# Optimization experiments

Hardware: AMD Instinct MI355X
Metric: run time of the kernel (lower is better)

The kernel has to match this reference:

```python
import jax, jax.numpy as jnp
import numpy as np

N_NODES = 100000
N_EDGES = 3200000
IN_DIM, HID, OUT = 512, 256, 64


def setup_inputs() -> dict:
    key = jax.random.key(0)
    k1, k2, k3, k4, k5, k6 = jax.random.split(key, 6)
    x = jax.random.normal(k1, (N_NODES, IN_DIM), dtype=jnp.float32)
    edge_src = jax.random.randint(k2, (N_EDGES,), 0, N_NODES, dtype=jnp.int32)
    edge_dst = jax.random.randint(k3, (N_EDGES,), 0, N_NODES, dtype=jnp.int32)
    edge_val = jax.random.uniform(k4, (N_EDGES,), dtype=jnp.float32)
    # glorot init as in the original `glorot([input_dim, output_dim])`
    w1 = jax.random.normal(k5, (IN_DIM, HID), dtype=jnp.float32) * np.sqrt(2.0 / (IN_DIM + HID))
    w2 = jax.random.normal(k6, (HID, OUT), dtype=jnp.float32) * np.sqrt(2.0 / (HID + OUT))
    return {"x": x, "edge_src": edge_src, "edge_dst": edge_dst,
            "edge_val": edge_val, "w1": w1, "w2": w2}


def _spmm(edge_src, edge_dst, edge_val, dense):
    # support @ dense : out[i] = sum_j A[i,j] * dense[j], A given as COO edges
    msgs = edge_val[:, None] * dense[edge_dst]            # [E, D] gather
    return jax.ops.segment_sum(msgs, edge_src, num_segments=N_NODES)  # scatter-add


def reference(x, edge_src, edge_dst, edge_val, w1, w2):
    # Layer 1: pre_sup = X @ W1 ; support = A @ pre_sup ; relu (no bias)
    h = jax.nn.relu(_spmm(edge_src, edge_dst, edge_val, x @ w1))  # [N, HID]
    # Layer 2: identity activation
    logits = _spmm(edge_src, edge_dst, edge_val, h @ w2)          # [N, OUT]
    return logits
```

## Files before the change

kernel.cpp:

```cpp
#include <hip/hip_runtime.h>

#define NN 100000
#define NE 3200000
#define IN_DIM 512
#define HID 256
#define OUTD 64
#define NB 196
#define CAP 20480
#define EPB 3125

typedef _Float16 f16x8 __attribute__((ext_vector_type(8)));
typedef float f32x4 __attribute__((ext_vector_type(4)));

__device__ __forceinline__ void async_copy16(void* lds, const void* g) {
    __builtin_amdgcn_global_load_lds(
        (const __attribute__((address_space(1))) void*)g,
        (__attribute__((address_space(3))) void*)lds, 16, 0, 0);
}

__device__ __forceinline__ void dq4(int w, float m, float* a) {
    int lo = (w & 0x00ff00ff) | 0x64006400;
    int hi = ((w >> 8) & 0x00ff00ff) | 0x64006400;
    asm("v_fma_mix_f32 %0, %1, %2, %0 op_sel:[0,0,0] op_sel_hi:[1,0,0]" : "+v"(a[0]) : "v"(lo), "v"(m));
    asm("v_fma_mix_f32 %0, %1, %2, %0 op_sel:[0,0,0] op_sel_hi:[1,0,0]" : "+v"(a[1]) : "v"(hi), "v"(m));
    asm("v_fma_mix_f32 %0, %1, %2, %0 op_sel:[1,0,0] op_sel_hi:[1,0,0]" : "+v"(a[2]) : "v"(lo), "v"(m));
    asm("v_fma_mix_f32 %0, %1, %2, %0 op_sel:[1,0,0] op_sel_hi:[1,0,0]" : "+v"(a[3]) : "v"(hi), "v"(m));
}


__global__ void prep_kernel(const float* __restrict__ w1, const float* __restrict__ w2,
                            _Float16* __restrict__ w1t, _Float16* __restrict__ w2t,
                            int* __restrict__ cursor) {
    int idx = blockIdx.x * blockDim.x + threadIdx.x;
    if (idx < NB) cursor[idx] = idx * CAP;
    if (idx < IN_DIM * HID) {
        int k = idx / HID, n = idx % HID;
        w1t[(size_t)n * IN_DIM + k] = (_Float16)w1[idx];
    } else if (idx < IN_DIM * HID + HID * OUTD) {
        int j = idx - IN_DIM * HID;
        int k = j / OUTD, n = j % OUTD;
        w2t[(size_t)n * HID + k] = (_Float16)w2[j];
    }
}


__global__ __launch_bounds__(256) void bin_kernel(const int* __restrict__ src,
                                                  const int* __restrict__ dst,
                                                  const float* __restrict__ val,
                                                  int* __restrict__ cursor,
                                                  int2* __restrict__ pairs_tmp,
                                                  int E) {
    __shared__ int s_src[EPB];
    __shared__ int s_dst[EPB];
    __shared__ int s_val[EPB];
    __shared__ int hist[NB];
    __shared__ int base[NB];
    const int t = threadIdx.x;
    const int lo = blockIdx.x * EPB;
    const int cnt = min(E - lo, EPB);
    for (int i = t; i < NB; i += 256) hist[i] = 0;
    for (int i = t; i < cnt; i += 256) {
        s_src[i] = src[lo + i];
        s_dst[i] = dst[lo + i];
        s_val[i] = __float_as_int(val[lo + i]);
    }
    __syncthreads();
    for (int i = t; i < cnt; i += 256) atomicAdd(&hist[s_src[i] >> 9], 1);
    __syncthreads();
    for (int i = t; i < NB; i += 256) {
        base[i] = atomicAdd(&cursor[i], hist[i]);
        hist[i] = 0;
    }
    __syncthreads();
    for (int i = t; i < cnt; i += 256) {
        int s = s_src[i];
        int b = s >> 9;
        int l = atomicAdd(&hist[b], 1);
        int pos = base[b] + l;
        pairs_tmp[pos] = make_int2(s_dst[i] | ((s & 511) << 20), s_val[i]);
    }
}


__global__ void bucket_scan_kernel(const int* __restrict__ cursor,
                                   int* __restrict__ bbase, int* __restrict__ offs) {
    __shared__ int sz[NB];
    int t = threadIdx.x;
    if (t < NB) sz[t] = cursor[t] - t * CAP;
    __syncthreads();
    if (t == 0) {
        int acc = 0;
        for (int i = 0; i < NB; ++i) { bbase[i] = acc; acc += sz[i]; }
        bbase[NB] = acc;
        offs[NN] = acc;
    }
}


#define CSR_LDS 18432
__global__ __launch_bounds__(1024) void csr_kernel(const int* __restrict__ cursor,
                                                   const int* __restrict__ bbase,
                                                   const int2* __restrict__ pairs_tmp,
                                                   const float* __restrict__ scales,
                                                   int* __restrict__ offs,
                                                   int2* __restrict__ pairs) {
    __shared__ int sx[CSR_LDS];
    __shared__ int sv[CSR_LDS];
    __shared__ int cnt[512];
    __shared__ int wsum[8];
    const int b = blockIdx.x;
    const int t = threadIdx.x;
    const int s0 = b << 9;
    const int base = bbase[b];
    const int n_b = cursor[b] - b * CAP;
    const int tlo = b * CAP;
    if (t < 512) cnt[t] = 0;
    __syncthreads();
    for (int i = t; i < n_b; i += 1024) {
        int2 pv = pairs_tmp[tlo + i];
        sx[i] = pv.x;
        sv[i] = pv.y;
        atomicAdd(&cnt[((unsigned)pv.x) >> 20], 1);
    }
    __syncthreads();
    int my = 0, incl = 0;
    if (t < 512) {
        my = cnt[t];
        incl = my;
        #pragma unroll
        for (int d = 1; d < 64; d <<= 1) {
            int y = __shfl_up(incl, d);
            if ((t & 63) >= d) incl += y;
        }
        if ((t & 63) == 63) wsum[t >> 6] = incl;
    }
    __syncthreads();
    if (t == 0) {
        int acc = 0;
        #pragma unroll
        for (int i = 0; i < 8; ++i) { int v = wsum[i]; wsum[i] = acc; acc += v; }
    }
    __syncthreads();
    if (t < 512) {
        int excl = base + incl - my + wsum[t >> 6];
        int s = s0 + t;
        if (s < NN) offs[s] = excl;
        cnt[t] = excl;
    }
    __syncthreads();
    for (int i = t; i < n_b; i += 1024) {
        int x = sx[i];
        int so = ((unsigned)x) >> 20;
        int p = atomicAdd(&cnt[so], 1);
        int dst = x & 0xFFFFF;
        float v = __int_as_float(sv[i]) * scales[dst];
        pairs[p] = make_int2(dst, __float_as_int(v));
    }
}


__global__ __launch_bounds__(256) void gemm1_f32a(const float* __restrict__ A,
                                                  const _Float16* __restrict__ Bt,
                                                  unsigned char* __restrict__ qC,
                                                  float* __restrict__ scales,
                                                  int M) {
    __shared__ float    As[2][64 * 32];
    __shared__ _Float16 Bs[2][256 * 32];
    __shared__ float    rmaxl[2][64];
    const int tid  = threadIdx.x;
    const int lane = tid & 63;
    const int wave = tid >> 6;
    const int wm = wave >> 1, wn = wave & 1;
    const int m0 = blockIdx.x * 64;

    f32x4 acc[2][8];
    #pragma unroll
    for (int i = 0; i < 2; ++i)
        #pragma unroll
        for (int j = 0; j < 8; ++j) acc[i][j] = (f32x4){0.f, 0.f, 0.f, 0.f};

    auto stage = [&](int b, int k0) {
        #pragma unroll
        for (int it = 0; it < 2; ++it) {
            int i = it * 256 + tid;
            int r = i >> 3;
            int cl = (i & 7) ^ (r & 7);
            int gr = m0 + r; if (gr >= M) gr = M - 1;
            async_copy16((char*)As[b] + i * 16, A + (size_t)gr * IN_DIM + k0 + cl * 4);
        }
        #pragma unroll
        for (int it = 0; it < 4; ++it) {
            int i = it * 256 + tid;
            int r = i >> 2;
            int cl = (i & 3) ^ (r & 3);
            async_copy16((char*)Bs[b] + i * 16, Bt + (size_t)r * IN_DIM + k0 + cl * 8);
        }
    };

    stage(0, 0);
    __syncthreads();

    int cur = 0;
    const int kc = lane >> 4;
    for (int t = 0; t < IN_DIM / 32; ++t) {
        if (t + 1 < IN_DIM / 32) stage(cur ^ 1, (t + 1) * 32);

        f16x8 af[2];
        #pragma unroll
        for (int m = 0; m < 2; ++m) {
            int r = wm * 32 + m * 16 + (lane & 15);
            int p0 = (2 * kc) ^ (r & 7);
            int p1 = (2 * kc + 1) ^ (r & 7);
            f32x4 c0 = *(const f32x4*)((const char*)As[cur] + r * 128 + p0 * 16);
            f32x4 c1 = *(const f32x4*)((const char*)As[cur] + r * 128 + p1 * 16);
            f16x8 v = { (_Float16)c0[0], (_Float16)c0[1], (_Float16)c0[2], (_Float16)c0[3],
                        (_Float16)c1[0], (_Float16)c1[1], (_Float16)c1[2], (_Float16)c1[3] };
            af[m] = v;
        }
        f16x8 bf[8];
        #pragma unroll
        for (int n = 0; n < 8; ++n) {
            int r = wn * 128 + n * 16 + (lane & 15);
            bf[n] = *(const f16x8*)((const char*)Bs[cur] + r * 64 + ((kc ^ (r & 3)) * 16));
        }
        #pragma unroll
        for (int m = 0; m < 2; ++m)
            #pragma unroll
            for (int n = 0; n < 8; ++n)
                acc[m][n] = __builtin_amdgcn_mfma_f32_16x16x32_f16(af[m], bf[n], acc[m][n], 0, 0, 0);

        __syncthreads();
        cur ^= 1;
    }

    #pragma unroll
    for (int m = 0; m < 2; ++m)
        #pragma unroll
        for (int r = 0; r < 4; ++r) {
            float mm = 0.f;
            #pragma unroll
            for (int n = 0; n < 8; ++n) mm = fmaxf(mm, fabsf(acc[m][n][r]));
            #pragma unroll
            for (int d = 1; d < 16; d <<= 1) mm = fmaxf(mm, __shfl_xor(mm, d));
            if ((lane & 15) == 0)
                rmaxl[wn][wm * 32 + m * 16 + kc * 4 + r] = mm;
        }
    __syncthreads();
    #pragma unroll
    for (int m = 0; m < 2; ++m)
        #pragma unroll
        for (int r = 0; r < 4; ++r) {
            int lrow = wm * 32 + m * 16 + kc * 4 + r;
            int row = m0 + lrow;
            float full = fmaxf(fmaxf(rmaxl[0][lrow], rmaxl[1][lrow]), 1e-12f);
            float inv = 127.0f / full;
            if (row < M) {
                #pragma unroll
                for (int n = 0; n < 8; ++n) {
                    int col = wn * 128 + n * 16 + (lane & 15);
                    qC[(size_t)row * HID + col] =
                        (unsigned char)(__float2int_rn(acc[m][n][r] * inv) + 128);
                }
                if (wn == 0 && (lane & 15) == 0) scales[row] = full * (1.0f / 127.0f);
            }
        }
}


__global__ __launch_bounds__(256) void spmm_relu_mm2(const int* __restrict__ offs,
                                                     const int2* __restrict__ pairs,
                                                     const unsigned char* __restrict__ qpre,
                                                     const float* __restrict__ scales,
                                                     const _Float16* __restrict__ w2t,
                                                     unsigned char* __restrict__ qh2,
                                                     float* __restrict__ ratio2, int n) {
    __shared__ __align__(16) char hl_raw[16 * 528];
    __shared__ float rmax2[4][16];
    const int tid  = threadIdx.x;
    const int lane = tid & 63;
    const int wid  = tid >> 6;
    const int par  = lane >> 4;
    const int fl   = lane & 15;
    const int nbase = blockIdx.x * 16;
    const unsigned char* qbase = qpre + fl * 16;

    #pragma unroll 1
    for (int i = 0; i < 4; ++i) {
        const int node = nbase + wid * 4 + i;
        const int beg = offs[node], end = offs[node + 1];
        float a[16] = {};
        float msum = 0.f;
        int k = beg;
        for (; k + 16 <= end; k += 16) {
            int2 pr[4];
            #pragma unroll
            for (int j = 0; j < 4; ++j) pr[j] = pairs[k + 4 * j + par];
            int4 qv[4];
            #pragma unroll
            for (int j = 0; j < 4; ++j)
                qv[j] = *(const int4*)(qbase + (size_t)pr[j].x * HID);
            #pragma unroll
            for (int j = 0; j < 4; ++j) {
                float m = __int_as_float(pr[j].y);
                msum += m;
                dq4(qv[j].x, m, a + 0);
                dq4(qv[j].y, m, a + 4);
                dq4(qv[j].z, m, a + 8);
                dq4(qv[j].w, m, a + 12);
            }
        }
        if (k < end) {
            int2 pr[4];
            float m_[4];
            #pragma unroll
            for (int j = 0; j < 4; ++j) {
                int idx = k + 4 * j + par;
                int cidx = idx < end ? idx : end - 1;
                pr[j] = pairs[cidx];
                m_[j] = idx < end ? __int_as_float(pr[j].y) : 0.f;
            }
            int4 qv[4];
            #pragma unroll
            for (int j = 0; j < 4; ++j)
                qv[j] = *(const int4*)(qbase + (size_t)pr[j].x * HID);
            #pragma unroll
            for (int j = 0; j < 4; ++j) {
                float m = m_[j];
                msum += m;
                dq4(qv[j].x, m, a + 0);
                dq4(qv[j].y, m, a + 4);
                dq4(qv[j].z, m, a + 8);
                dq4(qv[j].w, m, a + 12);
            }
        }
        #pragma unroll
        for (int q = 0; q < 16; ++q) {
            a[q] += __shfl_xor(a[q], 16);
            a[q] += __shfl_xor(a[q], 32);
        }
        msum += __shfl_xor(msum, 16);
        msum += __shfl_xor(msum, 32);
        if (par == 0) {
            float bias = 1152.f * msum;
            f16x8 o0, o1;
            #pragma unroll
            for (int q = 0; q < 8; ++q) {
                o0[q] = (_Float16)fmaxf(a[q] - bias, 0.f);
                o1[q] = (_Float16)fmaxf(a[8 + q] - bias, 0.f);
            }
            char* bp = hl_raw + (wid * 4 + i) * 528 + fl * 16;
            *(f16x8*)bp         = o0;
            *(f16x8*)(bp + 256) = o1;
        }
    }
    __syncthreads();

    const int r  = lane & 15;
    const int kc = lane >> 4;
    f32x4 acc = (f32x4){0.f, 0.f, 0.f, 0.f};
    #pragma unroll
    for (int kk = 0; kk < 8; ++kk) {
        int c = kk * 4 + kc;
        f16x8 af = *(const f16x8*)(hl_raw + r * 528 + ((c & 1) << 8) + ((c >> 1) << 4));
        f16x8 bf = *(const f16x8*)(w2t + (size_t)(wid * 16 + r) * HID + kk * 32 + kc * 8);
        acc = __builtin_amdgcn_mfma_f32_16x16x32_f16(af, bf, acc, 0, 0, 0);
    }
    float mxv[4];
    #pragma unroll
    for (int j = 0; j < 4; ++j) {
        float mm = fabsf(acc[j]);
        #pragma unroll
        for (int d = 1; d < 16; d <<= 1) mm = fmaxf(mm, __shfl_xor(mm, d));
        mxv[j] = mm;
    }
    if (r == 0) {
        #pragma unroll
        for (int j = 0; j < 4; ++j) rmax2[wid][kc * 4 + j] = mxv[j];
    }
    __syncthreads();
    #pragma unroll
    for (int j = 0; j < 4; ++j) {
        int ln = kc * 4 + j;
        int node = nbase + ln;
        float full = fmaxf(fmaxf(fmaxf(rmax2[0][ln], rmax2[1][ln]),
                                 fmaxf(rmax2[2][ln], rmax2[3][ln])), 1e-12f);
        qh2[(size_t)node * OUTD + wid * 16 + r] =
            (unsigned char)(__float2int_rn(acc[j] * (127.0f / full)) + 128);
        if (wid == 0 && r == 0)
            ratio2[node] = full * (1.0f / 127.0f) / scales[node];
    }
}


__global__ __launch_bounds__(256) void spmm64_q(const int* __restrict__ offs,
                                                const int2* __restrict__ pairs,
                                                const unsigned char* __restrict__ qh2,
                                                const float* __restrict__ ratio2,
                                                float* __restrict__ out, int n) {
    int node = blockIdx.x * 4 + (threadIdx.x >> 6);
    if (node >= n) return;
    int lane = threadIdx.x & 63;
    int par = lane >> 2;
    int fl  = lane & 3;
    int beg = offs[node], end = offs[node + 1];
    const unsigned char* qbase = qh2 + fl * 16;
    float a[16] = {};
    float msum = 0.f;
    int k = beg;
    for (; k + 32 <= end; k += 32) {
        int2 pr[2];
        #pragma unroll
        for (int j = 0; j < 2; ++j) pr[j] = pairs[k + 16 * j + par];
        float rt[2];
        #pragma unroll
        for (int j = 0; j < 2; ++j) rt[j] = ratio2[pr[j].x];
        int4 qv[2];
        #pragma unroll
        for (int j = 0; j < 2; ++j)
            qv[j] = *(const int4*)(qbase + (size_t)pr[j].x * OUTD);
        #pragma unroll
        for (int j = 0; j < 2; ++j) {
            float m = __int_as_float(pr[j].y) * rt[j];
            msum += m;
            dq4(qv[j].x, m, a + 0);
            dq4(qv[j].y, m, a + 4);
            dq4(qv[j].z, m, a + 8);
            dq4(qv[j].w, m, a + 12);
        }
    }
    if (k < end) {
        int2 pr[2];
        float m_[2];
        #pragma unroll
        for (int j = 0; j < 2; ++j) {
            int idx = k + 16 * j + par;
            int cidx = idx < end ? idx : end - 1;
            pr[j] = pairs[cidx];
            m_[j] = idx < end ? __int_as_float(pr[j].y) * ratio2[pr[j].x] : 0.f;
        }
        int4 qv[2];
        #pragma unroll
        for (int j = 0; j < 2; ++j)
            qv[j] = *(const int4*)(qbase + (size_t)pr[j].x * OUTD);
        #pragma unroll
        for (int j = 0; j < 2; ++j) {
            float m = m_[j];
            msum += m;
            dq4(qv[j].x, m, a + 0);
            dq4(qv[j].y, m, a + 4);
            dq4(qv[j].z, m, a + 8);
            dq4(qv[j].w, m, a + 12);
        }
    }
    #pragma unroll
    for (int q = 0; q < 16; ++q) {
        a[q] += __shfl_xor(a[q], 4);
        a[q] += __shfl_xor(a[q], 8);
        a[q] += __shfl_xor(a[q], 16);
        a[q] += __shfl_xor(a[q], 32);
    }
    msum += __shfl_xor(msum, 4);
    msum += __shfl_xor(msum, 8);
    msum += __shfl_xor(msum, 16);
    msum += __shfl_xor(msum, 32);
    if (par == 0) {
        float bias = 1152.f * msum;
        float* ob = out + (size_t)node * OUTD + fl * 16;
        #pragma unroll
        for (int c = 0; c < 4; ++c) {
            float4 o = make_float4(a[4 * c] - bias, a[4 * c + 1] - bias,
                                   a[4 * c + 2] - bias, a[4 * c + 3] - bias);
            *(float4*)(ob + 4 * c) = o;
        }
    }
}


extern "C" void kernel_launch(void* const* d_in, const int* in_sizes, int n_in,
                              void* d_out, int out_size, void* d_ws, size_t ws_size,
                              hipStream_t stream) {
    const float* x    = (const float*)d_in[0];
    const int*   esrc = (const int*)d_in[1];
    const int*   edst = (const int*)d_in[2];
    const float* eval = (const float*)d_in[3];
    const float* w1   = (const float*)d_in[4];
    const float* w2   = (const float*)d_in[5];
    float* out = (float*)d_out;

    char* ws = (char*)d_ws;
    unsigned char* qpre   = (unsigned char*)(ws + 0);
    unsigned char* qh2    = (unsigned char*)(ws + 25600000);
    float*        scales  = (float*)(ws + 32000000);
    float*        ratio2  = (float*)(ws + 32400000);
    int2*         pairs   = (int2*)(ws + 32800000);
    int2*         pairs_t = (int2*)(ws + 58400000);
    int*          cursor  = (int*)(ws + 90512640);
    int*          bbase   = (int*)(ws + 90513664);
    int*          offs    = (int*)(ws + 90514688);
    _Float16*     w1t     = (_Float16*)(ws + 90914816);
    _Float16*     w2t     = (_Float16*)(ws + 91176960);

    prep_kernel<<<(IN_DIM * HID + HID * OUTD + 255) / 256, 256, 0, stream>>>(w1, w2, w1t, w2t, cursor);

    bin_kernel<<<1024, 256, 0, stream>>>(esrc, edst, eval, cursor, pairs_t, NE);

    bucket_scan_kernel<<<1, 256, 0, stream>>>(cursor, bbase, offs);

    gemm1_f32a<<<(NN + 63) / 64, 256, 0, stream>>>(x, w1t, qpre, scales, NN);

    csr_kernel<<<NB, 1024, 0, stream>>>(cursor, bbase, pairs_t, scales, offs, pairs);

    spmm_relu_mm2<<<NN / 16, 256, 0, stream>>>(offs, pairs, qpre, scales, w2t, qh2, ratio2, NN);

    spmm64_q<<<(NN + 3) / 4, 256, 0, stream>>>(offs, pairs, qh2, ratio2, out, NN);
}
```

Baseline: 385.3 us.

## Store layer-2 intermediate as fp16 and drop LDS staging in bin/csr kernels

Layer-2 features are now written as fp16 prescaled by the inverse of the per-node layer-1 scale, replacing the int8 quantization with a per-row max reduction, a ratio array and a bias correction. The final SpMM gathers 16-byte fp16 chunks with 8 lanes per row and needs no bias subtraction, which also removes a block-wide sync in the fused kernel. The cost is twice the gather bytes per edge in the last SpMM. Separately, bin_kernel and csr_kernel stop staging dst/val in LDS and reread global memory instead, which cuts LDS use (more occupancy) at the price of extra global reads.

Result: slower. 397.3 us (+3.1%).

```diff
diff --git a/kernel.cpp b/kernel.cpp
--- a/kernel.cpp
+++ b/kernel.cpp
@@ -25,6 +25,11 @@
     asm("v_fma_mix_f32 %0, %1, %2, %0 op_sel:[0,0,0] op_sel_hi:[1,0,0]" : "+v"(a[1]) : "v"(hi), "v"(m));
     asm("v_fma_mix_f32 %0, %1, %2, %0 op_sel:[1,0,0] op_sel_hi:[1,0,0]" : "+v"(a[2]) : "v"(lo), "v"(m));
     asm("v_fma_mix_f32 %0, %1, %2, %0 op_sel:[1,0,0] op_sel_hi:[1,0,0]" : "+v"(a[3]) : "v"(hi), "v"(m));
+}
+
+__device__ __forceinline__ void dqh2(int w, float m, float* a0, float* a1) {
+    asm("v_fma_mix_f32 %0, %1, %2, %0 op_sel:[0,0,0] op_sel_hi:[1,0,0]" : "+v"(*a0) : "v"(w), "v"(m));
+    asm("v_fma_mix_f32 %0, %1, %2, %0 op_sel:[1,0,0] op_sel_hi:[1,0,0]" : "+v"(*a1) : "v"(w), "v"(m));
 }
 
 
@@ -51,19 +56,13 @@
                                                   int2* __restrict__ pairs_tmp,
                                                   int E) {
     __shared__ int s_src[EPB];
-    __shared__ int s_dst[EPB];
-    __shared__ int s_val[EPB];
     __shared__ int hist[NB];
     __shared__ int base[NB];
     const int t = threadIdx.x;
     const int lo = blockIdx.x * EPB;
     const int cnt = min(E - lo, EPB);
     for (int i = t; i < NB; i += 256) hist[i] = 0;
-    for (int i = t; i < cnt; i += 256) {
-        s_src[i] = src[lo + i];
-        s_dst[i] = dst[lo + i];
-        s_val[i] = __float_as_int(val[lo + i]);
-    }
+    for (int i = t; i < cnt; i += 256) s_src[i] = src[lo + i];
     __syncthreads();
     for (int i = t; i < cnt; i += 256) atomicAdd(&hist[s_src[i] >> 9], 1);
     __syncthreads();
@@ -77,7 +76,7 @@
         int b = s >> 9;
         int l = atomicAdd(&hist[b], 1);
         int pos = base[b] + l;
-        pairs_tmp[pos] = make_int2(s_dst[i] | ((s & 511) << 20), s_val[i]);
+        pairs_tmp[pos] = make_int2(dst[lo + i] | ((s & 511) << 20), __float_as_int(val[lo + i]));
     }
 }
 
@@ -97,15 +96,12 @@
 }
 
 
-#define CSR_LDS 18432
 __global__ __launch_bounds__(1024) void csr_kernel(const int* __restrict__ cursor,
                                                    const int* __restrict__ bbase,
                                                    const int2* __restrict__ pairs_tmp,
                                                    const float* __restrict__ scales,
                                                    int* __restrict__ offs,
                                                    int2* __restrict__ pairs) {
-    __shared__ int sx[CSR_LDS];
-    __shared__ int sv[CSR_LDS];
     __shared__ int cnt[512];
     __shared__ int wsum[8];
     const int b = blockIdx.x;
@@ -116,12 +112,8 @@
     const int tlo = b * CAP;
     if (t < 512) cnt[t] = 0;
     __syncthreads();
-    for (int i = t; i < n_b; i += 1024) {
-        int2 pv = pairs_tmp[tlo + i];
-        sx[i] = pv.x;
-        sv[i] = pv.y;
-        atomicAdd(&cnt[((unsigned)pv.x) >> 20], 1);
-    }
+    for (int i = t; i < n_b; i += 1024)
+        atomicAdd(&cnt[((unsigned)pairs_tmp[tlo + i].x) >> 20], 1);
     __syncthreads();
     int my = 0, incl = 0;
     if (t < 512) {
@@ -149,11 +141,11 @@
     }
     __syncthreads();
     for (int i = t; i < n_b; i += 1024) {
-        int x = sx[i];
-        int so = ((unsigned)x) >> 20;
+        int2 pv = pairs_tmp[tlo + i];
+        int so = ((unsigned)pv.x) >> 20;
         int p = atomicAdd(&cnt[so], 1);
-        int dst = x & 0xFFFFF;
-        float v = __int_as_float(sv[i]) * scales[dst];
+        int dst = pv.x & 0xFFFFF;
+        float v = __int_as_float(pv.y) * scales[dst];
         pairs[p] = make_int2(dst, __float_as_int(v));
     }
 }
@@ -272,10 +264,8 @@
                                                      const unsigned char* __restrict__ qpre,
                                                      const float* __restrict__ scales,
                                                      const _Float16* __restrict__ w2t,
-                                                     unsigned char* __restrict__ qh2,
-                                                     float* __restrict__ ratio2, int n) {
+                                                     _Float16* __restrict__ h2s, int n) {
     __shared__ __align__(16) char hl_raw[16 * 528];
-    __shared__ float rmax2[4][16];
     const int tid  = threadIdx.x;
     const int lane = tid & 63;
     const int wid  = tid >> 6;
@@ -365,113 +355,80 @@
         f16x8 bf = *(const f16x8*)(w2t + (size_t)(wid * 16 + r) * HID + kk * 32 + kc * 8);
         acc = __builtin_amdgcn_mfma_f32_16x16x32_f16(af, bf, acc, 0, 0, 0);
     }
-    float mxv[4];
     #pragma unroll
     for (int j = 0; j < 4; ++j) {
-        float mm = fabsf(acc[j]);
-        #pragma unroll
-        for (int d = 1; d < 16; d <<= 1) mm = fmaxf(mm, __shfl_xor(mm, d));
-        mxv[j] = mm;
-    }
-    if (r == 0) {
-        #pragma unroll
-        for (int j = 0; j < 4; ++j) rmax2[wid][kc * 4 + j] = mxv[j];
-    }
-    __syncthreads();
-    #pragma unroll
-    for (int j = 0; j < 4; ++j) {
-        int ln = kc * 4 + j;
-        int node = nbase + ln;
-        float full = fmaxf(fmaxf(fmaxf(rmax2[0][ln], rmax2[1][ln]),
-                                 fmaxf(rmax2[2][ln], rmax2[3][ln])), 1e-12f);
-        qh2[(size_t)node * OUTD + wid * 16 + r] =
-            (unsigned char)(__float2int_rn(acc[j] * (127.0f / full)) + 128);
-        if (wid == 0 && r == 0)
-            ratio2[node] = full * (1.0f / 127.0f) / scales[node];
+        int node = nbase + kc * 4 + j;
+        float inv = 1.0f / scales[node];
+        h2s[(size_t)node * OUTD + wid * 16 + r] = (_Float16)(acc[j] * inv);
     }
 }
 
 
 __global__ __launch_bounds__(256) void spmm64_q(const int* __restrict__ offs,
                                                 const int2* __restrict__ pairs,
-                                                const unsigned char* __restrict__ qh2,
-                                                const float* __restrict__ ratio2,
+                                                const _Float16* __restrict__ h2s,
                                                 float* __restrict__ out, int n) {
     int node = blockIdx.x * 4 + (threadIdx.x >> 6);
     if (node >= n) return;
     int lane = threadIdx.x & 63;
-    int par = lane >> 2;
-    int fl  = lane & 3;
+    int par = lane >> 3;
+    int fl  = lane & 7;
     int beg = offs[node], end = offs[node + 1];
-    const unsigned char* qbase = qh2 + fl * 16;
-    float a[16] = {};
-    float msum = 0.f;
+    const _Float16* qbase = h2s + fl * 8;
+    float a[8] = {};
     int k = beg;
     for (; k + 32 <= end; k += 32) {
-        int2 pr[2];
-        #pragma unroll
-        for (int j = 0; j < 2; ++j) pr[j] = pairs[k + 16 * j + par];
-        float rt[2];
-        #pragma unroll
-        for (int j = 0; j < 2; ++j) rt[j] = ratio2[pr[j].x];
-        int4 qv[2];
-        #pragma unroll
-        for (int j = 0; j < 2; ++j)
+        int2 pr[4];
+        #pragma unroll
+        for (int j = 0; j < 4; ++j) pr[j] = pairs[k + 8 * j + par];
+        int4 qv[4];
+        #pragma unroll
+        for (int j = 0; j < 4; ++j)
             qv[j] = *(const int4*)(qbase + (size_t)pr[j].x * OUTD);
         #pragma unroll
-        for (int j = 0; j < 2; ++j) {
-            float m = __int_as_float(pr[j].y) * rt[j];
-            msum += m;
-            dq4(qv[j].x, m, a + 0);
-            dq4(qv[j].y, m, a + 4);
-            dq4(qv[j].z, m, a + 8);
-            dq4(qv[j].w, m, a + 12);
+        for (int j = 0; j < 4; ++j) {
+            float m = __int_as_float(pr[j].y);
+            dqh2(qv[j].x, m, a + 0, a + 1);
+            dqh2(qv[j].y, m, a + 2, a + 3);
+            dqh2(qv[j].z, m, a + 4, a + 5);
+            dqh2(qv[j].w, m, a + 6, a + 7);
         }
     }
     if (k < end) {
-        int2 pr[2];
-        float m_[2];
-        #pragma unroll
-        for (int j = 0; j < 2; ++j) {
-            int idx = k + 16 * j + par;
+        int2 pr[4];
+        float m_[4];
+        #pragma unroll
+        for (int j = 0; j < 4; ++j) {
+            int idx = k + 8 * j + par;
             int cidx = idx < end ? idx : end - 1;
             pr[j] = pairs[cidx];
-            m_[j] = idx < end ? __int_as_float(pr[j].y) * ratio2[pr[j].x] : 0.f;
-        }
-        int4 qv[2];
-        #pragma unroll
-        for (int j = 0; j < 2; ++j)
+            m_[j] = idx < end ? __int_as_float(pr[j].y) : 0.f;
+        }
+        int4 qv[4];
+        #pragma unroll
+        for (int j = 0; j < 4; ++j)
             qv[j] = *(const int4*)(qbase + (size_t)pr[j].x * OUTD);
         #pragma unroll
-        for (int j = 0; j < 2; ++j) {
+        for (int j = 0; j < 4; ++j) {
             float m = m_[j];
-            msum += m;
-            dq4(qv[j].x, m, a + 0);
-            dq4(qv[j].y, m, a + 4);
-            dq4(qv[j].z, m, a + 8);
-            dq4(qv[j].w, m, a + 12);
-        }
-    }
-    #pragma unroll
-    for (int q = 0; q < 16; ++q) {
-        a[q] += __shfl_xor(a[q], 4);
+            dqh2(qv[j].x, m, a + 0, a + 1);
+            dqh2(qv[j].y, m, a + 2, a + 3);
+            dqh2(qv[j].z, m, a + 4, a + 5);
+            dqh2(qv[j].w, m, a + 6, a + 7);
+        }
+    }
+    #pragma unroll
+    for (int q = 0; q < 8; ++q) {
         a[q] += __shfl_xor(a[q], 8);
         a[q] += __shfl_xor(a[q], 16);
         a[q] += __shfl_xor(a[q], 32);
     }
-    msum += __shfl_xor(msum, 4);
-    msum += __shfl_xor(msum, 8);
-    msum += __shfl_xor(msum, 16);
-    msum += __shfl_xor(msum, 32);
     if (par == 0) {
-        float bias = 1152.f * msum;
-        float* ob = out + (size_t)node * OUTD + fl * 16;
-        #pragma unroll
-        for (int c = 0; c < 4; ++c) {
-            float4 o = make_float4(a[4 * c] - bias, a[4 * c + 1] - bias,
-                                   a[4 * c + 2] - bias, a[4 * c + 3] - bias);
-            *(float4*)(ob + 4 * c) = o;
-        }
+        float* ob = out + (size_t)node * OUTD + fl * 8;
+        float4 o0 = make_float4(a[0], a[1], a[2], a[3]);
+        float4 o1 = make_float4(a[4], a[5], a[6], a[7]);
+        *(float4*)ob       = o0;
+        *(float4*)(ob + 4) = o1;
     }
 }
 
@@ -489,16 +446,15 @@
 
     char* ws = (char*)d_ws;
     unsigned char* qpre   = (unsigned char*)(ws + 0);
-    unsigned char* qh2    = (unsigned char*)(ws + 25600000);
-    float*        scales  = (float*)(ws + 32000000);
-    float*        ratio2  = (float*)(ws + 32400000);
-    int2*         pairs   = (int2*)(ws + 32800000);
-    int2*         pairs_t = (int2*)(ws + 58400000);
-    int*          cursor  = (int*)(ws + 90512640);
-    int*          bbase   = (int*)(ws + 90513664);
-    int*          offs    = (int*)(ws + 90514688);
-    _Float16*     w1t     = (_Float16*)(ws + 90914816);
-    _Float16*     w2t     = (_Float16*)(ws + 91176960);
+    _Float16*     h2s     = (_Float16*)(ws + 25600000);
+    float*        scales  = (float*)(ws + 38400000);
+    int2*         pairs   = (int2*)(ws + 38800000);
+    int2*         pairs_t = (int2*)(ws + 64400000);
+    int*          cursor  = (int*)(ws + 96512640);
+    int*          bbase   = (int*)(ws + 96513664);
+    int*          offs    = (int*)(ws + 96514688);
+    _Float16*     w1t     = (_Float16*)(ws + 96914816);
+    _Float16*     w2t     = (_Float16*)(ws + 97176960);
 
     prep_kernel<<<(IN_DIM * HID + HID * OUTD + 255) / 256, 256, 0, stream>>>(w1, w2, w1t, w2t, cursor);
 
@@ -510,7 +466,7 @@
 
     csr_kernel<<<NB, 1024, 0, stream>>>(cursor, bbase, pairs_t, scales, offs, pairs);
 
-    spmm_relu_mm2<<<NN / 16, 256, 0, stream>>>(offs, pairs, qpre, scales, w2t, qh2, ratio2, NN);
-
-    spmm64_q<<<(NN + 3) / 4, 256, 0, stream>>>(offs, pairs, qh2, ratio2, out, NN);
-}
+    spmm_relu_mm2<<<NN / 16, 256, 0, stream>>>(offs, pairs, qpre, scales, w2t, h2s, NN);
+
+    spmm64_q<<<(NN + 3) / 4, 256, 0, stream>>>(offs, pairs, h2s, out, NN);
+}
```

## Fuse edge binning and first GEMM into one interleaved launch

Applied to the files above, without the earlier changes.

Merges the edge-binning kernel and the X@W1 GEMM into a single kernel whose blocks are interleaved 3:2 between GEMM tiles and binning chunks. The compute-bound GEMM then overlaps with the memory and atomic-bound binning, and one launch is removed. The binning body now keeps only src in LDS and reads dst/val directly from global memory. The CSR kernel drops its large LDS staging and reads pairs_tmp twice from global. The cost is higher LDS per block for the binning blocks (sized for the GEMM) and extra global reads in the CSR pass.

New measurement: 371.1 us. 3.7% less time.

```diff
diff --git a/kernel.cpp b/kernel.cpp
--- a/kernel.cpp
+++ b/kernel.cpp
@@ -8,6 +8,10 @@
 #define NB 196
 #define CAP 20480
 #define EPB 3125
+#define G1_BLOCKS 1563
+#define BIN_BLOCKS 1024
+#define MEGA_GRID 2605
+#define MEGA_LDS 49664
 
 typedef _Float16 f16x8 __attribute__((ext_vector_type(8)));
 typedef float f32x4 __attribute__((ext_vector_type(4)));
@@ -44,134 +48,19 @@
 }
 
 
-__global__ __launch_bounds__(256) void bin_kernel(const int* __restrict__ src,
-                                                  const int* __restrict__ dst,
-                                                  const float* __restrict__ val,
-                                                  int* __restrict__ cursor,
-                                                  int2* __restrict__ pairs_tmp,
-                                                  int E) {
-    __shared__ int s_src[EPB];
-    __shared__ int s_dst[EPB];
-    __shared__ int s_val[EPB];
-    __shared__ int hist[NB];
-    __shared__ int base[NB];
-    const int t = threadIdx.x;
-    const int lo = blockIdx.x * EPB;
-    const int cnt = min(E - lo, EPB);
-    for (int i = t; i < NB; i += 256) hist[i] = 0;
-    for (int i = t; i < cnt; i += 256) {
-        s_src[i] = src[lo + i];
-        s_dst[i] = dst[lo + i];
-        s_val[i] = __float_as_int(val[lo + i]);
-    }
-    __syncthreads();
-    for (int i = t; i < cnt; i += 256) atomicAdd(&hist[s_src[i] >> 9], 1);
-    __syncthreads();
-    for (int i = t; i < NB; i += 256) {
-        base[i] = atomicAdd(&cursor[i], hist[i]);
-        hist[i] = 0;
-    }
-    __syncthreads();
-    for (int i = t; i < cnt; i += 256) {
-        int s = s_src[i];
-        int b = s >> 9;
-        int l = atomicAdd(&hist[b], 1);
-        int pos = base[b] + l;
-        pairs_tmp[pos] = make_int2(s_dst[i] | ((s & 511) << 20), s_val[i]);
-    }
-}
-
-
-__global__ void bucket_scan_kernel(const int* __restrict__ cursor,
-                                   int* __restrict__ bbase, int* __restrict__ offs) {
-    __shared__ int sz[NB];
-    int t = threadIdx.x;
-    if (t < NB) sz[t] = cursor[t] - t * CAP;
-    __syncthreads();
-    if (t == 0) {
-        int acc = 0;
-        for (int i = 0; i < NB; ++i) { bbase[i] = acc; acc += sz[i]; }
-        bbase[NB] = acc;
-        offs[NN] = acc;
-    }
-}
-
-
-#define CSR_LDS 18432
-__global__ __launch_bounds__(1024) void csr_kernel(const int* __restrict__ cursor,
-                                                   const int* __restrict__ bbase,
-                                                   const int2* __restrict__ pairs_tmp,
-                                                   const float* __restrict__ scales,
-                                                   int* __restrict__ offs,
-                                                   int2* __restrict__ pairs) {
-    __shared__ int sx[CSR_LDS];
-    __shared__ int sv[CSR_LDS];
-    __shared__ int cnt[512];
-    __shared__ int wsum[8];
-    const int b = blockIdx.x;
-    const int t = threadIdx.x;
-    const int s0 = b << 9;
-    const int base = bbase[b];
-    const int n_b = cursor[b] - b * CAP;
-    const int tlo = b * CAP;
-    if (t < 512) cnt[t] = 0;
-    __syncthreads();
-    for (int i = t; i < n_b; i += 1024) {
-        int2 pv = pairs_tmp[tlo + i];
-        sx[i] = pv.x;
-        sv[i] = pv.y;
-        atomicAdd(&cnt[((unsigned)pv.x) >> 20], 1);
-    }
-    __syncthreads();
-    int my = 0, incl = 0;
-    if (t < 512) {
-        my = cnt[t];
-        incl = my;
-        #pragma unroll
-        for (int d = 1; d < 64; d <<= 1) {
-            int y = __shfl_up(incl, d);
-            if ((t & 63) >= d) incl += y;
-        }
-        if ((t & 63) == 63) wsum[t >> 6] = incl;
-    }
-    __syncthreads();
-    if (t == 0) {
-        int acc = 0;
-        #pragma unroll
-        for (int i = 0; i < 8; ++i) { int v = wsum[i]; wsum[i] = acc; acc += v; }
-    }
-    __syncthreads();
-    if (t < 512) {
-        int excl = base + incl - my + wsum[t >> 6];
-        int s = s0 + t;
-        if (s < NN) offs[s] = excl;
-        cnt[t] = excl;
-    }
-    __syncthreads();
-    for (int i = t; i < n_b; i += 1024) {
-        int x = sx[i];
-        int so = ((unsigned)x) >> 20;
-        int p = atomicAdd(&cnt[so], 1);
-        int dst = x & 0xFFFFF;
-        float v = __int_as_float(sv[i]) * scales[dst];
-        pairs[p] = make_int2(dst, __float_as_int(v));
-    }
-}
-
-
-__global__ __launch_bounds__(256) void gemm1_f32a(const float* __restrict__ A,
-                                                  const _Float16* __restrict__ Bt,
-                                                  unsigned char* __restrict__ qC,
-                                                  float* __restrict__ scales,
-                                                  int M) {
-    __shared__ float    As[2][64 * 32];
-    __shared__ _Float16 Bs[2][256 * 32];
-    __shared__ float    rmaxl[2][64];
+__device__ void gemm1_body(char* smem, int bx,
+                           const float* __restrict__ A,
+                           const _Float16* __restrict__ Bt,
+                           unsigned char* __restrict__ qC,
+                           float* __restrict__ scales, int M) {
+    float    (*As)[64 * 32]  = (float(*)[64 * 32])smem;
+    _Float16 (*Bs)[256 * 32] = (_Float16(*)[256 * 32])(smem + 16384);
+    float    (*rmaxl)[64]    = (float(*)[64])(smem + 49152);
     const int tid  = threadIdx.x;
     const int lane = tid & 63;
     const int wave = tid >> 6;
     const int wm = wave >> 1, wn = wave & 1;
-    const int m0 = blockIdx.x * 64;
+    const int m0 = bx * 64;
 
     f32x4 acc[2][8];
     #pragma unroll
@@ -264,6 +153,128 @@
                 if (wn == 0 && (lane & 15) == 0) scales[row] = full * (1.0f / 127.0f);
             }
         }
+}
+
+__device__ void bin_body(char* smem, int bx,
+                         const int* __restrict__ src,
+                         const int* __restrict__ dst,
+                         const float* __restrict__ val,
+                         int* __restrict__ cursor,
+                         int2* __restrict__ pairs_tmp, int E) {
+    int* s_src = (int*)smem;
+    int* hist  = (int*)(smem + 12500);
+    int* base  = (int*)(smem + 13284);
+    const int t = threadIdx.x;
+    const int lo = bx * EPB;
+    const int cnt = min(E - lo, EPB);
+    for (int i = t; i < NB; i += 256) hist[i] = 0;
+    for (int i = t; i < cnt; i += 256) s_src[i] = src[lo + i];
+    __syncthreads();
+    for (int i = t; i < cnt; i += 256) atomicAdd(&hist[s_src[i] >> 9], 1);
+    __syncthreads();
+    for (int i = t; i < NB; i += 256) {
+        base[i] = atomicAdd(&cursor[i], hist[i]);
+        hist[i] = 0;
+    }
+    __syncthreads();
+    for (int i = t; i < cnt; i += 256) {
+        int s = s_src[i];
+        int b = s >> 9;
+        int l = atomicAdd(&hist[b], 1);
+        int pos = base[b] + l;
+        pairs_tmp[pos] = make_int2(dst[lo + i] | ((s & 511) << 20), __float_as_int(val[lo + i]));
+    }
+}
+
+__global__ __launch_bounds__(256) void mega1(const float* __restrict__ x,
+                                             const _Float16* __restrict__ w1t,
+                                             unsigned char* __restrict__ qpre,
+                                             float* __restrict__ scales,
+                                             const int* __restrict__ src,
+                                             const int* __restrict__ dst,
+                                             const float* __restrict__ val,
+                                             int* __restrict__ cursor,
+                                             int2* __restrict__ pairs_tmp) {
+    __shared__ __align__(16) char smem[MEGA_LDS];
+    const int b = blockIdx.x;
+    const int phase = b % 5;
+    if (phase < 3) {
+        int g = (b / 5) * 3 + phase;
+        if (g < G1_BLOCKS) gemm1_body(smem, g, x, w1t, qpre, scales, NN);
+    } else {
+        int bb = (b / 5) * 2 + (phase - 3);
+        if (bb < BIN_BLOCKS) bin_body(smem, bb, src, dst, val, cursor, pairs_tmp, NE);
+    }
+}
+
+
+__global__ void bucket_scan_kernel(const int* __restrict__ cursor,
+                                   int* __restrict__ bbase, int* __restrict__ offs) {
+    __shared__ int sz[NB];
+    int t = threadIdx.x;
+    if (t < NB) sz[t] = cursor[t] - t * CAP;
+    __syncthreads();
+    if (t == 0) {
+        int acc = 0;
+        for (int i = 0; i < NB; ++i) { bbase[i] = acc; acc += sz[i]; }
+        bbase[NB] = acc;
+        offs[NN] = acc;
+    }
+}
+
+
+__global__ __launch_bounds__(1024) void csr_kernel(const int* __restrict__ cursor,
+                                                   const int* __restrict__ bbase,
+                                                   const int2* __restrict__ pairs_tmp,
+                                                   const float* __restrict__ scales,
+                                                   int* __restrict__ offs,
+                                                   int2* __restrict__ pairs) {
+    __shared__ int cnt[512];
+    __shared__ int wsum[8];
+    const int b = blockIdx.x;
+    const int t = threadIdx.x;
+    const int s0 = b << 9;
+    const int base = bbase[b];
+    const int n_b = cursor[b] - b * CAP;
+    const int tlo = b * CAP;
+    if (t < 512) cnt[t] = 0;
+    __syncthreads();
+    for (int i = t; i < n_b; i += 1024)
+        atomicAdd(&cnt[((unsigned)pairs_tmp[tlo + i].x) >> 20], 1);
+    __syncthreads();
+    int my = 0, incl = 0;
+    if (t < 512) {
+        my = cnt[t];
+        incl = my;
+        #pragma unroll
+        for (int d = 1; d < 64; d <<= 1) {
+            int y = __shfl_up(incl, d);
+            if ((t & 63) >= d) incl += y;
+        }
+        if ((t & 63) == 63) wsum[t >> 6] = incl;
+    }
+    __syncthreads();
+    if (t == 0) {
+        int acc = 0;
+        #pragma unroll
+        for (int i = 0; i < 8; ++i) { int v = wsum[i]; wsum[i] = acc; acc += v; }
+    }
+    __syncthreads();
+    if (t < 512) {
+        int excl = base + incl - my + wsum[t >> 6];
+        int s = s0 + t;
+        if (s < NN) offs[s] = excl;
+        cnt[t] = excl;
+    }
+    __syncthreads();
+    for (int i = t; i < n_b; i += 1024) {
+        int2 pv = pairs_tmp[tlo + i];
+        int so = ((unsigned)pv.x) >> 20;
+        int p = atomicAdd(&cnt[so], 1);
+        int dst = pv.x & 0xFFFFF;
+        float v = __int_as_float(pv.y) * scales[dst];
+        pairs[p] = make_int2(dst, __float_as_int(v));
+    }
 }
 
 
@@ -502,12 +513,10 @@
 
     prep_kernel<<<(IN_DIM * HID + HID * OUTD + 255) / 256, 256, 0, stream>>>(w1, w2, w1t, w2t, cursor);
 
-    bin_kernel<<<1024, 256, 0, stream>>>(esrc, edst, eval, cursor, pairs_t, NE);
+    mega1<<<MEGA_GRID, 256, 0, stream>>>(x, w1t, qpre, scales, esrc, edst, eval, cursor, pairs_t);
 
     bucket_scan_kernel<<<1, 256, 0, stream>>>(cursor, bbase, offs);
 
-    gemm1_f32a<<<(NN + 63) / 64, 256, 0, stream>>>(x, w1t, qpre, scales, NN);
-
     csr_kernel<<<NB, 1024, 0, stream>>>(cursor, bbase, pairs_t, scales, offs, pairs);
 
     spmm_relu_mm2<<<NN / 16, 256, 0, stream>>>(offs, pairs, qpre, scales, w2t, qh2, ratio2, NN);
```
